# Optimization experiments

Hardware: AMD Instinct MI355X
Metric: run time of the kernel (lower is better)

The kernel has to match this reference:

```python
import jax, jax.numpy as jnp
import numpy as np

MONOTONICITY = 1.0  # init kwarg monotonicity=1


def _interp_channel(xq, xs, ys):
    """Monotonic piecewise-linear interp for one channel.
    xq: (N,) query points; xs: (B,) sorted breakpoints; ys: (B,) knot values.
    Linear extrapolation beyond both ends using the edge segment slopes.
    """
    B = xs.shape[0]
    # segment index in [1, B-1]; elements below xs[0] / above xs[-1] use edge segments
    idx = jnp.clip(jnp.searchsorted(xs, xq), 1, B - 1)
    x0 = xs[idx - 1]
    x1 = xs[idx]
    y0 = ys[idx - 1]
    y1 = ys[idx]
    slope = (y1 - y0) / (x1 - x0)
    return y0 + slope * (xq - x0)


def setup_inputs() -> dict:
    key = jax.random.key(0)
    k1, k2, k3, k4 = jax.random.split(key, 4)
    N, C, B = 2097152, 16, 32
    x = jax.random.normal(k1, (N, C), dtype=jnp.float32)
    # learned parameters of MonoPointPWL (per channel)
    xp = jax.random.normal(k2, (C, B), dtype=jnp.float32)        # raw x positions (sorted at use)
    y0 = jax.random.normal(k3, (C,), dtype=jnp.float32)          # y value at first knot
    dy = jax.random.normal(k4, (C, B - 1), dtype=jnp.float32)    # raw segment deltas
    return {"x": x, "xp": xp, "y0": y0, "dy": dy}


def reference(x, xp, y0, dy):
    # sorted breakpoint x positions per channel: (C, B)
    xs = jnp.sort(xp, axis=1)
    # monotone knot values: y0 + cumsum(|dy|) * monotonicity, (C, B)
    steps = jnp.abs(dy) * MONOTONICITY
    ys = y0[:, None] + jnp.concatenate(
        [jnp.zeros_like(y0)[:, None], jnp.cumsum(steps, axis=1)], axis=1
    )
    # vectorize over channels: x is (N, C), params are (C, B)
    out = jax.vmap(_interp_channel, in_axes=(1, 0, 0), out_axes=1)(x, xs, ys)
    return out
```

## Files before the change

### kernel.cpp

```cpp
#include <hip/hip_runtime.h>
#include <hip/hip_bf16.h>


#define C_CH 16
#define B_KN 32
#define COPIES 16
#define TAB_WORDS (96 * 4 * COPIES)

typedef float f4v __attribute__((ext_vector_type(4)));


__global__ __launch_bounds__(512) void pwl_setup_kernel(
    const float* __restrict__ xp, const float* __restrict__ y0,
    const float* __restrict__ dy, float* __restrict__ ws) {
    __shared__ float s_x[C_CH][B_KN];
    __shared__ float s_xs[C_CH][B_KN];
    __shared__ float s_ys[C_CH][B_KN];
    int t = threadIdx.x;
    int c = t >> 5;
    int k = t & 31;
    float v = xp[c * B_KN + k];
    s_x[c][k] = v;
    __syncthreads();
    int rank = 0;
#pragma unroll
    for (int j = 0; j < B_KN; ++j) {
        float u = s_x[c][j];
        rank += (u < v || (u == v && j < k)) ? 1 : 0;
    }
    s_xs[c][rank] = v;
    float acc = y0[c];
    for (int j = 0; j < k; ++j) acc += fabsf(dy[c * (B_KN - 1) + j]);
    s_ys[c][k] = acc;
    __syncthreads();
    ws[c * B_KN + k] = s_xs[c][k];
    if (k < B_KN - 1) {
        float x0 = s_xs[c][k], x1 = s_xs[c][k + 1];
        float ya = s_ys[c][k], yb = s_ys[c][k + 1];
        float a = (yb - ya) / (x1 - x0);
        float b = ya - a * x0;
        ws[512 + c * B_KN + k]  = a;
        ws[1024 + c * B_KN + k] = b;
    } else {
        ws[512 + c * B_KN + k]  = 0.0f;
        ws[1024 + c * B_KN + k] = 0.0f;
    }
}

__global__ __launch_bounds__(512) void pwl_main_kernel(
    const float4* __restrict__ x, float4* __restrict__ out,
    const float* __restrict__ ws, int n4) {
    __shared__ float s_tab[TAB_WORDS];
    int t = threadIdx.x;
    for (int w = t; w < TAB_WORDS; w += 512) {
        int cp = w & 15;
        int r  = w >> 4;
        int m  = r / 96;
        int tt = r - m * 96;
        int arr = tt >> 5;
        int idx = tt & 31;
        int c = ((cp & 3) << 2) + m;
        s_tab[w] = ws[arr * 512 + c * 32 + idx];
    }
    int c0 = (t & 3) << 2;
    float v15[4], v7[4], v23[4], v3[4], v11[4], v19[4], v27[4];
#pragma unroll
    for (int j = 0; j < 4; ++j) {
        const float* xs = ws + (c0 + j) * B_KN;
        v15[j] = xs[15];
        v7[j]  = xs[7];
        v23[j] = xs[23];
        v3[j]  = xs[3];
        v11[j] = xs[11];
        v19[j] = xs[19];
        v27[j] = xs[27];
    }
    __syncthreads();

    int cp = t & 15;
    int tid = blockIdx.x * 512 + t;
    int total = gridDim.x * 512;

    for (int i = tid; i < n4; i += 2 * total) {
        int i1 = i + total;
        float4 v0 = x[i];
        float4 v1 = (i1 < n4) ? x[i1] : v0;
        float xv[8] = {v0.x, v0.y, v0.z, v0.w, v1.x, v1.y, v1.z, v1.w};
        float rr[8];
#pragma unroll
        for (int u = 0; u < 8; ++u) {
            int j = u & 3;
            float xq = xv[u];
            bool b16 = (v15[j] < xq);
            float l2v = b16 ? v23[j] : v7[j];
            bool b8 = (l2v < xq);
            float l3a = b16 ? v19[j] : v3[j];
            float l3b = b16 ? v27[j] : v11[j];
            float l3v = b8 ? l3b : l3a;
            bool b4 = (l3v < xq);
            int pos = (b16 ? 16 : 0) + (b8 ? 8 : 0) + (b4 ? 4 : 0);
            float w1 = s_tab[((j * 96 + (pos + 1)) << 4) | cp];
            pos += (w1 < xq) ? 2 : 0;
            float w2 = s_tab[((j * 96 + pos) << 4) | cp];
            pos += (w2 < xq) ? 1 : 0;
            int seg = pos < 2 ? 0 : (pos > 31 ? 30 : pos - 1);
            float a = s_tab[((j * 96 + 32 + seg) << 4) | cp];
            float b = s_tab[((j * 96 + 64 + seg) << 4) | cp];
            rr[u] = fmaf(a, xq, b);
        }
        f4v r0 = {rr[0], rr[1], rr[2], rr[3]};
        __builtin_nontemporal_store(r0, (f4v*)&out[i]);
        if (i1 < n4) {
            f4v r1 = {rr[4], rr[5], rr[6], rr[7]};
            __builtin_nontemporal_store(r1, (f4v*)&out[i1]);
        }
    }
}

extern "C" void kernel_launch(void* const* d_in, const int* in_sizes, int n_in,
                              void* d_out, int out_size, void* d_ws, size_t ws_size,
                              hipStream_t stream) {
    const float* x  = (const float*)d_in[0];
    const float* xp = (const float*)d_in[1];
    const float* y0 = (const float*)d_in[2];
    const float* dy = (const float*)d_in[3];
    float* out = (float*)d_out;
    float* ws  = (float*)d_ws;

    pwl_setup_kernel<<<1, 512, 0, stream>>>(xp, y0, dy, ws);

    int n4 = in_sizes[0] / 4;
    int blocks = 1024;
    pwl_main_kernel<<<blocks, 512, 0, stream>>>((const float4*)x, (float4*)out, ws, n4);
}
```

Measured before the change: 58.68 us.

## Fuse table setup into main kernel and pack lookup table with vector LDS reads

Drops the separate single-block setup kernel. Every block of the main kernel now sorts the breakpoints, builds the cumulative y values and the slope/intercept table in shared memory itself, so one launch and the global workspace round trip go away. The lookup table is no longer replicated 16 times. Breakpoints are stored rotated per channel so the last two binary-search steps use a single float4 LDS read, and slope and intercept are packed as a float2 so one read fetches both. The cost is redundant setup work in all 2048 blocks (a 32-step rank sort and a serial cumsum that reads dy from global memory) and possible LDS bank conflicts now that the table is no longer replicated.

```diff
diff --git a/kernel.cpp b/kernel.cpp
--- a/kernel.cpp
+++ b/kernel.cpp
@@ -4,69 +4,58 @@
 
 #define C_CH 16
 #define B_KN 32
-#define COPIES 16
-#define TAB_WORDS (96 * 4 * COPIES)
 
 typedef float f4v __attribute__((ext_vector_type(4)));
 
+__global__ __launch_bounds__(256) void pwl_fused_kernel(
+    const float4* __restrict__ x, float4* __restrict__ out,
+    const float* __restrict__ xp, const float* __restrict__ y0,
+    const float* __restrict__ dy, int n4) {
+    __shared__ float  s_raw[C_CH][B_KN];
+    __shared__ float  s_xs[C_CH][B_KN];
+    __shared__ float  s_ys[C_CH][B_KN];
+    __shared__ float  s_x4[C_CH * B_KN];
+    __shared__ float2 s_ab[C_CH * B_KN];
 
-__global__ __launch_bounds__(512) void pwl_setup_kernel(
-    const float* __restrict__ xp, const float* __restrict__ y0,
-    const float* __restrict__ dy, float* __restrict__ ws) {
-    __shared__ float s_x[C_CH][B_KN];
-    __shared__ float s_xs[C_CH][B_KN];
-    __shared__ float s_ys[C_CH][B_KN];
     int t = threadIdx.x;
-    int c = t >> 5;
-    int k = t & 31;
-    float v = xp[c * B_KN + k];
-    s_x[c][k] = v;
+#pragma unroll
+    for (int p = t; p < 512; p += 256) s_raw[p >> 5][p & 31] = xp[p];
     __syncthreads();
-    int rank = 0;
 #pragma unroll
-    for (int j = 0; j < B_KN; ++j) {
-        float u = s_x[c][j];
-        rank += (u < v || (u == v && j < k)) ? 1 : 0;
+    for (int p = t; p < 512; p += 256) {
+        int c = p >> 5, k = p & 31;
+        float v = s_raw[c][k];
+        int rank = 0;
+#pragma unroll
+        for (int j = 0; j < B_KN; ++j) {
+            float u = s_raw[c][j];
+            rank += (u < v || (u == v && j < k)) ? 1 : 0;
+        }
+        s_xs[c][rank] = v;
+        float acc = y0[c];
+        for (int j = 0; j < k; ++j) acc += fabsf(dy[c * (B_KN - 1) + j]);
+        s_ys[c][k] = acc;
     }
-    s_xs[c][rank] = v;
-    float acc = y0[c];
-    for (int j = 0; j < k; ++j) acc += fabsf(dy[c * (B_KN - 1) + j]);
-    s_ys[c][k] = acc;
     __syncthreads();
-    ws[c * B_KN + k] = s_xs[c][k];
-    if (k < B_KN - 1) {
-        float x0 = s_xs[c][k], x1 = s_xs[c][k + 1];
-        float ya = s_ys[c][k], yb = s_ys[c][k + 1];
-        float a = (yb - ya) / (x1 - x0);
-        float b = ya - a * x0;
-        ws[512 + c * B_KN + k]  = a;
-        ws[1024 + c * B_KN + k] = b;
-    } else {
-        ws[512 + c * B_KN + k]  = 0.0f;
-        ws[1024 + c * B_KN + k] = 0.0f;
-    }
-}
-
-__global__ __launch_bounds__(512) void pwl_main_kernel(
-    const float4* __restrict__ x, float4* __restrict__ out,
-    const float* __restrict__ ws, int n4) {
-    __shared__ float s_tab[TAB_WORDS];
-    int t = threadIdx.x;
-    for (int w = t; w < TAB_WORDS; w += 512) {
-        int cp = w & 15;
-        int r  = w >> 4;
-        int m  = r / 96;
-        int tt = r - m * 96;
-        int arr = tt >> 5;
-        int idx = tt & 31;
-        int c = ((cp & 3) << 2) + m;
-        s_tab[w] = ws[arr * 512 + c * 32 + idx];
+#pragma unroll
+    for (int p = t; p < 512; p += 256) {
+        int c = p >> 5, k = p & 31;
+        float xk = s_xs[c][k];
+        s_x4[c * 32 + ((k + 4 * c) & 31)] = xk;
+        float a = 0.0f, b = 0.0f;
+        if (k < B_KN - 1) {
+            float ya = s_ys[c][k], yb = s_ys[c][k + 1];
+            a = (yb - ya) / (s_xs[c][k + 1] - xk);
+            b = ya - a * xk;
+        }
+        s_ab[c * 32 + ((k + c) & 31)] = make_float2(a, b);
     }
     int c0 = (t & 3) << 2;
     float v15[4], v7[4], v23[4], v3[4], v11[4], v19[4], v27[4];
+    __syncthreads();
 #pragma unroll
     for (int j = 0; j < 4; ++j) {
-        const float* xs = ws + (c0 + j) * B_KN;
+        const float* xs = s_xs[c0 + j];
         v15[j] = xs[15];
         v7[j]  = xs[7];
         v23[j] = xs[23];
@@ -75,11 +64,10 @@
         v19[j] = xs[19];
         v27[j] = xs[27];
     }
-    __syncthreads();
 
-    int cp = t & 15;
-    int tid = blockIdx.x * 512 + t;
-    int total = gridDim.x * 512;
+    const f4v* x4t = (const f4v*)s_x4;
+    int tid = blockIdx.x * 256 + t;
+    int total = gridDim.x * 256;
 
     for (int i = tid; i < n4; i += 2 * total) {
         int i1 = i + total;
@@ -90,6 +78,7 @@
 #pragma unroll
         for (int u = 0; u < 8; ++u) {
             int j = u & 3;
+            int c = c0 + j;
             float xq = xv[u];
             bool b16 = (v15[j] < xq);
             float l2v = b16 ? v23[j] : v7[j];
@@ -99,14 +88,14 @@
             float l3v = b8 ? l3b : l3a;
             bool b4 = (l3v < xq);
             int pos = (b16 ? 16 : 0) + (b8 ? 8 : 0) + (b4 ? 4 : 0);
-            float w1 = s_tab[((j * 96 + (pos + 1)) << 4) | cp];
-            pos += (w1 < xq) ? 2 : 0;
-            float w2 = s_tab[((j * 96 + pos) << 4) | cp];
-            pos += (w2 < xq) ? 1 : 0;
+            f4v w = x4t[c * 8 + (((pos + 4 * c) & 31) >> 2)];
+            bool b2 = (w.y < xq);
+            pos += b2 ? 2 : 0;
+            float wf = b2 ? w.z : w.x;
+            pos += (wf < xq) ? 1 : 0;
             int seg = pos < 2 ? 0 : (pos > 31 ? 30 : pos - 1);
-            float a = s_tab[((j * 96 + 32 + seg) << 4) | cp];
-            float b = s_tab[((j * 96 + 64 + seg) << 4) | cp];
-            rr[u] = fmaf(a, xq, b);
+            float2 ab = s_ab[c * 32 + ((seg + c) & 31)];
+            rr[u] = fmaf(ab.x, xq, ab.y);
         }
         f4v r0 = {rr[0], rr[1], rr[2], rr[3]};
         __builtin_nontemporal_store(r0, (f4v*)&out[i]);
@@ -125,11 +114,8 @@
     const float* y0 = (const float*)d_in[2];
     const float* dy = (const float*)d_in[3];
     float* out = (float*)d_out;
-    float* ws  = (float*)d_ws;
-
-    pwl_setup_kernel<<<1, 512, 0, stream>>>(xp, y0, dy, ws);
 
     int n4 = in_sizes[0] / 4;
-    int blocks = 1024;
-    pwl_main_kernel<<<blocks, 512, 0, stream>>>((const float4*)x, (float4*)out, ws, n4);
+    pwl_fused_kernel<<<2048, 256, 0, stream>>>((const float4*)x, (float4*)out,
+                                               xp, y0, dy, n4);
 }
```

After: 62.93 us. 7.2% more time.

## Replace replicated interleaved LDS table with padded per-channel arrays, 256-thread blocks

Applied to the files above, without the earlier changes.

Drops the 16-way replicated, bank-interleaved shared-memory lookup table and uses three padded [16][33] arrays for breakpoints, slopes and intercepts. This shrinks the LDS footprint and per-block table-fill cost. Lookups now index by channel and data-dependent position, which can cause more bank conflicts across lanes. Block size also changes from 512 to 256 threads, with the grid doubled to keep the same total thread count.

```diff
diff --git a/kernel.cpp b/kernel.cpp
--- a/kernel.cpp
+++ b/kernel.cpp
@@ -4,8 +4,6 @@
 
 #define C_CH 16
 #define B_KN 32
-#define COPIES 16
-#define TAB_WORDS (96 * 4 * COPIES)
 
 typedef float f4v __attribute__((ext_vector_type(4)));
 
@@ -47,20 +45,18 @@
     }
 }
 
-__global__ __launch_bounds__(512) void pwl_main_kernel(
+__global__ __launch_bounds__(256) void pwl_main_kernel(
     const float4* __restrict__ x, float4* __restrict__ out,
     const float* __restrict__ ws, int n4) {
-    __shared__ float s_tab[TAB_WORDS];
+    __shared__ float s_xs[C_CH][B_KN + 1];
+    __shared__ float s_a[C_CH][B_KN + 1];
+    __shared__ float s_b[C_CH][B_KN + 1];
     int t = threadIdx.x;
-    for (int w = t; w < TAB_WORDS; w += 512) {
-        int cp = w & 15;
-        int r  = w >> 4;
-        int m  = r / 96;
-        int tt = r - m * 96;
-        int arr = tt >> 5;
-        int idx = tt & 31;
-        int c = ((cp & 3) << 2) + m;
-        s_tab[w] = ws[arr * 512 + c * 32 + idx];
+    for (int p = t; p < C_CH * B_KN; p += 256) {
+        int c = p >> 5, k = p & 31;
+        s_xs[c][k] = ws[p];
+        s_a[c][k]  = ws[512 + p];
+        s_b[c][k]  = ws[1024 + p];
     }
     int c0 = (t & 3) << 2;
     float v15[4], v7[4], v23[4], v3[4], v11[4], v19[4], v27[4];
@@ -77,9 +73,8 @@
     }
     __syncthreads();
 
-    int cp = t & 15;
-    int tid = blockIdx.x * 512 + t;
-    int total = gridDim.x * 512;
+    int tid = blockIdx.x * 256 + t;
+    int total = gridDim.x * 256;
 
     for (int i = tid; i < n4; i += 2 * total) {
         int i1 = i + total;
@@ -90,6 +85,7 @@
 #pragma unroll
         for (int u = 0; u < 8; ++u) {
             int j = u & 3;
+            int c = c0 + j;
             float xq = xv[u];
             bool b16 = (v15[j] < xq);
             float l2v = b16 ? v23[j] : v7[j];
@@ -99,14 +95,10 @@
             float l3v = b8 ? l3b : l3a;
             bool b4 = (l3v < xq);
             int pos = (b16 ? 16 : 0) + (b8 ? 8 : 0) + (b4 ? 4 : 0);
-            float w1 = s_tab[((j * 96 + (pos + 1)) << 4) | cp];
-            pos += (w1 < xq) ? 2 : 0;
-            float w2 = s_tab[((j * 96 + pos) << 4) | cp];
-            pos += (w2 < xq) ? 1 : 0;
+            pos += (s_xs[c][pos + 1] < xq) ? 2 : 0;
+            pos += (s_xs[c][pos] < xq) ? 1 : 0;
             int seg = pos < 2 ? 0 : (pos > 31 ? 30 : pos - 1);
-            float a = s_tab[((j * 96 + 32 + seg) << 4) | cp];
-            float b = s_tab[((j * 96 + 64 + seg) << 4) | cp];
-            rr[u] = fmaf(a, xq, b);
+            rr[u] = fmaf(s_a[c][seg], xq, s_b[c][seg]);
         }
         f4v r0 = {rr[0], rr[1], rr[2], rr[3]};
         __builtin_nontemporal_store(r0, (f4v*)&out[i]);
@@ -130,6 +122,5 @@
     pwl_setup_kernel<<<1, 512, 0, stream>>>(xp, y0, dy, ws);
 
     int n4 = in_sizes[0] / 4;
-    int blocks = 1024;
-    pwl_main_kernel<<<blocks, 512, 0, stream>>>((const float4*)x, (float4*)out, ws, n4);
+    pwl_main_kernel<<<2048, 256, 0, stream>>>((const float4*)x, (float4*)out, ws, n4);
 }
```

Result: faster. 56.16 us (-4.3%).
